# Kernel optimization log

Hardware: AMD Instinct MI355X
Metric: run time of the kernel (lower is better)

Reference implementation:

```python
import math
import jax, jax.numpy as jnp
import numpy as np

B, S, H, D = 2, 8192, 16, 128
W = 4  # conv_kernel_size


def setup_inputs() -> dict:
    key = jax.random.key(0)
    ks = jax.random.split(key, 5)
    return {
        "q": jax.random.normal(ks[0], (B, S, H * D), dtype=jnp.float32),
        "k": jax.random.normal(ks[1], (B, S, H * D), dtype=jnp.float32),
        "v": jax.random.normal(ks[2], (B, S, H * D), dtype=jnp.float32),
        "a": jax.random.normal(ks[3], (B, S, H), dtype=jnp.float32),
        "b": jax.random.normal(ks[4], (B, S, H), dtype=jnp.float32),
        "head_dim": D,
        "conv_kernel_size": W,
    }


def reference(q, k, v, a, b, head_dim, conv_kernel_size):
    batch, seq_len, _ = q.shape
    kv_heads = k.shape[-1] // head_dim
    qh = q.reshape(batch, seq_len, kv_heads, head_dim)
    kh = k.reshape(batch, seq_len, kv_heads, head_dim)
    vh = v.reshape(batch, seq_len, kv_heads, head_dim)
    ah = a.reshape(batch, seq_len, kv_heads, 1)
    bh = b.reshape(batch, seq_len, kv_heads, 1)
    scale = 1.0 / math.sqrt(head_dim)

    out = jnp.zeros_like(vh)
    # For each offset delta, j = i - delta; padded (j<0) positions have k=v=0,
    # so their contribution (q.k)*gate*v is exactly zero.
    for delta in range(conv_kernel_size + 1):
        pad = ((0, 0), (delta, 0), (0, 0), (0, 0))
        kd = jnp.pad(kh, pad)[:, :seq_len]
        vd = jnp.pad(vh, pad)[:, :seq_len]
        bd = jnp.pad(bh, pad)[:, :seq_len]
        w = jnp.sum(qh * kd, axis=-1, keepdims=True) * scale  # [B,S,H,1]
        g = jax.nn.sigmoid(ah * bd)
        out = out + w * g * vd
    # position 0 is special-cased in the original: output = v_0 (no attention)
    out = out.at[:, 0].set(vh[:, 0])
    return out.reshape(batch, seq_len, -1)
```

## Files before the change

kernel.cpp:

```cpp
#include <hip/hip_runtime.h>
#include <math.h>

constexpr int B = 2;
constexpr int S = 8192;
constexpr int H = 16;
constexpr int D = 128;
constexpr int W = 4;
constexpr int HD = H * D;
constexpr float SCALE = 0.08838834764831845f;

template <int CTRL>
__device__ __forceinline__ float dpp_xadd(float x) {
    int r = __builtin_amdgcn_update_dpp(0, __float_as_int(x), CTRL, 0xF, 0xF, false);
    return x + __int_as_float(r);
}

__device__ __forceinline__ float group_reduce16(float p) {
    p = dpp_xadd<0xB1>(p);
    p = dpp_xadd<0x4E>(p);
    p = dpp_xadd<0x141>(p);
    p = dpp_xadd<0x140>(p);
    return p;
}

__device__ __forceinline__ float dot8(const float4& qa, const float4& qb,
                                      const float4& ka, const float4& kb) {
    return qa.x * ka.x + qa.y * ka.y + qa.z * ka.z + qa.w * ka.w +
           qb.x * kb.x + qb.y * kb.y + qb.z * kb.z + qb.w * kb.w;
}

__global__ __launch_bounds__(256, 4) void gdr_kernel(
    const float* __restrict__ q, const float* __restrict__ k,
    const float* __restrict__ v, const float* __restrict__ a,
    const float* __restrict__ b, float* __restrict__ out)
{
    const int tid  = threadIdx.x;
    const int h    = tid >> 4;
    const int lane = tid & 15;

    const int bid = blockIdx.x;
    const int xcd = bid & 7;
    const int j   = bid >> 3;
    const int c   = j & 1023;
    const int bb  = j >> 10;
    const int s   = xcd * (S / 8) + c;

    const int bs  = bb * S + s;
    const int row = bs * H + h;
    const int e   = row * D + lane * 4;

    if (s == 0) {
        *(float4*)(out + e)      = *(const float4*)(v + e);
        *(float4*)(out + e + 64) = *(const float4*)(v + e + 64);
        return;
    }

    const float4 qa = *(const float4*)(q + e);
    const float4 qb = *(const float4*)(q + e + 64);
    const float  ai = a[row];

    float4 acca = make_float4(0.f, 0.f, 0.f, 0.f);
    float4 accb = make_float4(0.f, 0.f, 0.f, 0.f);

    if (s >= W) {
        float4 ka[W + 1], kb[W + 1], va[W + 1], vb[W + 1];
        float  bg[W + 1];
#pragma unroll
        for (int d = 0; d <= W; ++d) {
            const int ee = e - d * HD;
            ka[d] = *(const float4*)(k + ee);
            kb[d] = *(const float4*)(k + ee + 64);
            va[d] = *(const float4*)(v + ee);
            vb[d] = *(const float4*)(v + ee + 64);
            bg[d] = b[row - d * H];
        }
#pragma unroll
        for (int d = 0; d <= W; ++d) {
            float p = dot8(qa, qb, ka[d], kb[d]);
            p = group_reduce16(p);
            const float g  = __builtin_amdgcn_rcpf(1.0f + __expf(-(ai * bg[d])));
            const float wg = p * SCALE * g;
            acca.x += wg * va[d].x; acca.y += wg * va[d].y;
            acca.z += wg * va[d].z; acca.w += wg * va[d].w;
            accb.x += wg * vb[d].x; accb.y += wg * vb[d].y;
            accb.z += wg * vb[d].z; accb.w += wg * vb[d].w;
        }
    } else {
        for (int d = 0; d <= s; ++d) {
            const int ee = e - d * HD;
            const float4 k4a = *(const float4*)(k + ee);
            const float4 k4b = *(const float4*)(k + ee + 64);
            const float4 v4a = *(const float4*)(v + ee);
            const float4 v4b = *(const float4*)(v + ee + 64);
            float p = dot8(qa, qb, k4a, k4b);
            p = group_reduce16(p);
            const float bj = b[row - d * H];
            const float g  = __builtin_amdgcn_rcpf(1.0f + __expf(-(ai * bj)));
            const float wg = p * SCALE * g;
            acca.x += wg * v4a.x; acca.y += wg * v4a.y;
            acca.z += wg * v4a.z; acca.w += wg * v4a.w;
            accb.x += wg * v4b.x; accb.y += wg * v4b.y;
            accb.z += wg * v4b.z; accb.w += wg * v4b.w;
        }
    }

    *(float4*)(out + e)      = acca;
    *(float4*)(out + e + 64) = accb;
}

extern "C" void kernel_launch(void* const* d_in, const int* in_sizes, int n_in,
                              void* d_out, int out_size, void* d_ws, size_t ws_size,
                              hipStream_t stream) {
    const float* q = (const float*)d_in[0];
    const float* k = (const float*)d_in[1];
    const float* v = (const float*)d_in[2];
    const float* a = (const float*)d_in[3];
    const float* b = (const float*)d_in[4];
    float* out = (float*)d_out;

    const int blocks = B * S;
    gdr_kernel<<<blocks, 256, 0, stream>>>(q, k, v, a, b, out);
}
```

Before: 421.8 us.

## Tile 64 positions per head into LDS via async global-to-LDS loads with split waits

Each block now handles one head across 64 consecutive positions, staging the 68-row K and V window (with a 4-row halo) in LDS through direct global-to-LDS loads. Each K/V row is then read from global memory about once instead of five times. The loads are issued in two halves, and the first two output groups are computed after only the first half has arrived, so compute overlaps the remaining loads. The cost is heavier LDS use, lower occupancy, and manual waitcnt bookkeeping that must stay in step with the number of issued loads.

```diff
diff --git a/kernel.cpp b/kernel.cpp
--- a/kernel.cpp
+++ b/kernel.cpp
@@ -1,5 +1,6 @@
 #include <hip/hip_runtime.h>
 #include <math.h>
+#include <stdint.h>
 
 constexpr int B = 2;
 constexpr int S = 8192;
@@ -7,14 +8,17 @@
 constexpr int D = 128;
 constexpr int W = 4;
 constexpr int HD = H * D;
+constexpr int TS = 64;
+constexpr int TR = TS + W;
+constexpr int SPLIT = 36;
 constexpr float SCALE = 0.08838834764831845f;
+constexpr int LDS_BYTES = TR * D * 4 * 2;
 
 template <int CTRL>
 __device__ __forceinline__ float dpp_xadd(float x) {
     int r = __builtin_amdgcn_update_dpp(0, __float_as_int(x), CTRL, 0xF, 0xF, false);
     return x + __int_as_float(r);
 }
-
 __device__ __forceinline__ float group_reduce16(float p) {
     p = dpp_xadd<0xB1>(p);
     p = dpp_xadd<0x4E>(p);
@@ -22,90 +26,141 @@
     p = dpp_xadd<0x140>(p);
     return p;
 }
-
 __device__ __forceinline__ float dot8(const float4& qa, const float4& qb,
                                       const float4& ka, const float4& kb) {
     return qa.x * ka.x + qa.y * ka.y + qa.z * ka.z + qa.w * ka.w +
            qb.x * kb.x + qb.y * kb.y + qb.z * kb.z + qb.w * kb.w;
 }
 
-__global__ __launch_bounds__(256, 4) void gdr_kernel(
+typedef const __attribute__((address_space(1))) uint32_t cg_u32;
+typedef __attribute__((address_space(3))) uint32_t lds_u32;
+__device__ __forceinline__ void gload_lds16(const float* g, float* l) {
+    __builtin_amdgcn_global_load_lds((cg_u32*)g, (lds_u32*)l, 16, 0, 0);
+}
+
+__device__ __forceinline__ void compute_row(
+    const float (*k_t)[D], const float (*v_t)[D], int r, int l4,
+    float4 qa, float4 qb, float ai, const float* bj,
+    float* outp, bool isS0)
+{
+    float4 acca = make_float4(0.f, 0.f, 0.f, 0.f);
+    float4 accb = make_float4(0.f, 0.f, 0.f, 0.f);
+    float4 v0a = acca, v0b = accb;
+#pragma unroll
+    for (int d = 0; d <= W; ++d) {
+        const int lr = r + W - d;
+        const float4 ka = *(const float4*)&k_t[lr][l4];
+        const float4 kb = *(const float4*)&k_t[lr][l4 + 64];
+        const float4 va = *(const float4*)&v_t[lr][l4];
+        const float4 vb = *(const float4*)&v_t[lr][l4 + 64];
+        float p = group_reduce16(dot8(qa, qb, ka, kb));
+        const float g  = __builtin_amdgcn_rcpf(1.0f + __expf(-(ai * bj[d])));
+        const float wg = p * SCALE * g;
+        acca.x += wg * va.x; acca.y += wg * va.y;
+        acca.z += wg * va.z; acca.w += wg * va.w;
+        accb.x += wg * vb.x; accb.y += wg * vb.y;
+        accb.z += wg * vb.z; accb.w += wg * vb.w;
+        if (d == 0) { v0a = va; v0b = vb; }
+    }
+    if (isS0) { acca = v0a; accb = v0b; }
+    *(float4*)outp        = acca;
+    *(float4*)(outp + 64) = accb;
+}
+
+__global__ __launch_bounds__(256, 2) void gdr_kernel(
     const float* __restrict__ q, const float* __restrict__ k,
     const float* __restrict__ v, const float* __restrict__ a,
     const float* __restrict__ b, float* __restrict__ out)
 {
+    extern __shared__ __align__(16) float smem[];
+    float (*k_t)[D] = (float (*)[D])smem;
+    float (*v_t)[D] = (float (*)[D])(smem + TR * D);
+
     const int tid  = threadIdx.x;
-    const int h    = tid >> 4;
-    const int lane = tid & 15;
+    const int wave = tid >> 6;
+    const int lane = tid & 63;
+    const int grp  = tid >> 4;
+    const int l4   = (tid & 15) * 4;
 
     const int bid = blockIdx.x;
     const int xcd = bid & 7;
-    const int j   = bid >> 3;
-    const int c   = j & 1023;
-    const int bb  = j >> 10;
-    const int s   = xcd * (S / 8) + c;
+    int t = bid >> 3;
+    const int c  = t & 15;  t >>= 4;
+    const int h  = t & 15;
+    const int bb = t >> 4;
+    const int s0 = xcd * (S / 8) + c * TS;
 
-    const int bs  = bb * S + s;
-    const int row = bs * H + h;
-    const int e   = row * D + lane * 4;
+    const int sA = s0 + grp;
+    const int sB = sA + 16;
+    const int sC = sA + 32;
+    const int sD = sA + 48;
 
-    if (s == 0) {
-        *(float4*)(out + e)      = *(const float4*)(v + e);
-        *(float4*)(out + e + 64) = *(const float4*)(v + e + 64);
-        return;
+    const int rowH = bb * S * H + h;
+    const int eA = (rowH + sA * H) * D + l4;
+    const int eB = eA + 16 * HD;
+    const int eC = eA + 32 * HD;
+    const int eD = eA + 48 * HD;
+
+    const float4 qaA = *(const float4*)(q + eA), qbA = *(const float4*)(q + eA + 64);
+    const float4 qaB = *(const float4*)(q + eB), qbB = *(const float4*)(q + eB + 64);
+    const float  aiA = a[rowH + sA * H], aiB = a[rowH + sB * H];
+    float bjA[W + 1], bjB[W + 1];
+#pragma unroll
+    for (int d = 0; d <= W; ++d) {
+        const int jA = (sA - d) < 0 ? 0 : (sA - d);
+        bjA[d] = b[rowH + jA * H];
+        bjB[d] = b[rowH + (sB - d) * H];
     }
 
-    const float4 qa = *(const float4*)(q + e);
-    const float4 qb = *(const float4*)(q + e + 64);
-    const float  ai = a[row];
+    if (s0 == 0 && tid < 128) {
+        const float4 z = make_float4(0.f, 0.f, 0.f, 0.f);
+        ((float4*)k_t)[tid] = z;
+        ((float4*)v_t)[tid] = z;
+    }
+    __builtin_amdgcn_sched_barrier(0);
 
-    float4 acca = make_float4(0.f, 0.f, 0.f, 0.f);
-    float4 accb = make_float4(0.f, 0.f, 0.f, 0.f);
-
-    if (s >= W) {
-        float4 ka[W + 1], kb[W + 1], va[W + 1], vb[W + 1];
-        float  bg[W + 1];
+    const int g0 = (rowH + (s0 - 4 + (lane >> 5)) * H) * D + (lane & 31) * 4;
+    const int pSkip = (s0 == 0) ? 2 : 0;
 #pragma unroll
-        for (int d = 0; d <= W; ++d) {
-            const int ee = e - d * HD;
-            ka[d] = *(const float4*)(k + ee);
-            kb[d] = *(const float4*)(k + ee + 64);
-            va[d] = *(const float4*)(v + ee);
-            vb[d] = *(const float4*)(v + ee + 64);
-            bg[d] = b[row - d * H];
-        }
-#pragma unroll
-        for (int d = 0; d <= W; ++d) {
-            float p = dot8(qa, qb, ka[d], kb[d]);
-            p = group_reduce16(p);
-            const float g  = __builtin_amdgcn_rcpf(1.0f + __expf(-(ai * bg[d])));
-            const float wg = p * SCALE * g;
-            acca.x += wg * va[d].x; acca.y += wg * va[d].y;
-            acca.z += wg * va[d].z; acca.w += wg * va[d].w;
-            accb.x += wg * vb[d].x; accb.y += wg * vb[d].y;
-            accb.z += wg * vb[d].z; accb.w += wg * vb[d].w;
-        }
-    } else {
-        for (int d = 0; d <= s; ++d) {
-            const int ee = e - d * HD;
-            const float4 k4a = *(const float4*)(k + ee);
-            const float4 k4b = *(const float4*)(k + ee + 64);
-            const float4 v4a = *(const float4*)(v + ee);
-            const float4 v4b = *(const float4*)(v + ee + 64);
-            float p = dot8(qa, qb, k4a, k4b);
-            p = group_reduce16(p);
-            const float bj = b[row - d * H];
-            const float g  = __builtin_amdgcn_rcpf(1.0f + __expf(-(ai * bj)));
-            const float wg = p * SCALE * g;
-            acca.x += wg * v4a.x; acca.y += wg * v4a.y;
-            acca.z += wg * v4a.z; acca.w += wg * v4a.w;
-            accb.x += wg * v4b.x; accb.y += wg * v4b.y;
-            accb.z += wg * v4b.z; accb.w += wg * v4b.w;
+    for (int p0 = 0; p0 < 5; ++p0) {
+        const int p = wave + 4 * p0;
+        if (p < 18 && p >= pSkip) {
+            gload_lds16(k + g0 + 2 * p * HD, &k_t[2 * p][0]);
+            gload_lds16(v + g0 + 2 * p * HD, &v_t[2 * p][0]);
         }
     }
+    __builtin_amdgcn_sched_barrier(0);
+#pragma unroll
+    for (int p0 = 0; p0 < 4; ++p0) {
+        const int r0 = SPLIT + 2 * (wave + 4 * p0);
+        gload_lds16(k + g0 + r0 * HD, &k_t[r0][0]);
+        gload_lds16(v + g0 + r0 * HD, &v_t[r0][0]);
+    }
+    __builtin_amdgcn_sched_barrier(0);
 
-    *(float4*)(out + e)      = acca;
-    *(float4*)(out + e + 64) = accb;
+    asm volatile("s_waitcnt vmcnt(8) lgkmcnt(0)" ::: "memory");
+    __builtin_amdgcn_s_barrier();
+    __builtin_amdgcn_sched_barrier(0);
+
+    const float4 qaC = *(const float4*)(q + eC), qbC = *(const float4*)(q + eC + 64);
+    const float4 qaD = *(const float4*)(q + eD), qbD = *(const float4*)(q + eD + 64);
+    const float  aiC = a[rowH + sC * H], aiD = a[rowH + sD * H];
+    float bjC[W + 1], bjD[W + 1];
+#pragma unroll
+    for (int d = 0; d <= W; ++d) {
+        bjC[d] = b[rowH + (sC - d) * H];
+        bjD[d] = b[rowH + (sD - d) * H];
+    }
+
+    compute_row(k_t, v_t, grp,      l4, qaA, qbA, aiA, bjA, out + eA, sA == 0);
+    compute_row(k_t, v_t, grp + 16, l4, qaB, qbB, aiB, bjB, out + eB, false);
+
+    asm volatile("s_waitcnt vmcnt(0)" ::: "memory");
+    __builtin_amdgcn_s_barrier();
+    __builtin_amdgcn_sched_barrier(0);
+
+    compute_row(k_t, v_t, grp + 32, l4, qaC, qbC, aiC, bjC, out + eC, false);
+    compute_row(k_t, v_t, grp + 48, l4, qaD, qbD, aiD, bjD, out + eD, false);
 }
 
 extern "C" void kernel_launch(void* const* d_in, const int* in_sizes, int n_in,
@@ -118,6 +173,6 @@
     const float* b = (const float*)d_in[4];
     float* out = (float*)d_out;
 
-    const int blocks = B * S;
-    gdr_kernel<<<blocks, 256, 0, stream>>>(q, k, v, a, b, out);
+    const int blocks = B * H * (S / TS);
+    gdr_kernel<<<blocks, 256, LDS_BYTES, stream>>>(q, k, v, a, b, out);
 }
```

Result: faster. 393.5 us (-6.7%).
